# Kernel optimization log

Hardware: AMD Instinct MI355X
Metric: run time of the kernel (lower is better)

The kernel has to match this reference:

```python
import jax, jax.numpy as jnp
import numpy as np

EPS_BN = 1e-5
EPS_LN = 1e-5
OUT_H, OUT_W = 256, 256


def conv2d(x, w, b, pad):
    y = jax.lax.conv_general_dilated(x, w, (1, 1), [(pad, pad), (pad, pad)],
                                     dimension_numbers=('NCHW', 'OIHW', 'NCHW'))
    return y + b[None, :, None, None]


def leaky(x):
    return jnp.where(x >= 0, x, 0.2 * x)


def bn_eval(x, g, b):
    # fresh BatchNorm2d in eval mode: running_mean=0, running_var=1
    scale = g / jnp.sqrt(1.0 + EPS_BN)
    return x * scale[None, :, None, None] + b[None, :, None, None]


def resize_bilinear(x, oh, ow):
    # align_corners=True bilinear, separable gathers
    n, c, h, w = x.shape
    sy = jnp.arange(oh, dtype=x.dtype) * ((h - 1) / (oh - 1))
    sx = jnp.arange(ow, dtype=x.dtype) * ((w - 1) / (ow - 1))
    y0 = jnp.clip(jnp.floor(sy).astype(jnp.int32), 0, h - 2)
    x0 = jnp.clip(jnp.floor(sx).astype(jnp.int32), 0, w - 2)
    fy = (sy - y0.astype(x.dtype))[None, None, :, None]
    fx = (sx - x0.astype(x.dtype))[None, None, None, :]
    top = x[:, :, y0, :] * (1 - fy) + x[:, :, y0 + 1, :] * fy        # (n,c,oh,w)
    out = top[:, :, :, x0] * (1 - fx) + top[:, :, :, x0 + 1] * fx    # (n,c,oh,ow)
    return out


def layernorm(x, g, b):
    mu = jnp.mean(x, axis=-1, keepdims=True)
    var = jnp.mean((x - mu) ** 2, axis=-1, keepdims=True)
    return (x - mu) * jax.lax.rsqrt(var + EPS_LN) * g + b


def setup_inputs() -> dict:
    key = jax.random.key(0)
    ks = iter(jax.random.split(key, 64))

    def rn(shape, scale=0.05):
        return (jax.random.normal(next(ks), shape, dtype=jnp.float32) * scale)

    inp = {'x': jax.random.normal(next(ks), (8, 64, 128, 128), dtype=jnp.float32)}
    inp.update(
        r_c7a_w=rn((16, 64, 7, 7)), r_c7a_b=jnp.zeros((16,), jnp.float32),
        r_c1_w=rn((16, 16, 1, 1)), r_c1_b=jnp.zeros((16,), jnp.float32),
        r_bn1_g=1.0 + rn((16,), 0.1), r_bn1_b=jnp.zeros((16,), jnp.float32),
        rb_c1_w=rn((16, 16, 3, 3)), rb_c1_b=jnp.zeros((16,), jnp.float32),
        rb_bn1_g=1.0 + rn((16,), 0.1), rb_bn1_b=jnp.zeros((16,), jnp.float32),
        rb_c2_w=rn((16, 16, 3, 3)), rb_c2_b=jnp.zeros((16,), jnp.float32),
        rb_bn2_g=1.0 + rn((16,), 0.1), rb_bn2_b=jnp.zeros((16,), jnp.float32),
        r_c3_w=rn((16, 16, 3, 3)), r_c3_b=jnp.zeros((16,), jnp.float32),
        r_bn2_g=1.0 + rn((16,), 0.1), r_bn2_b=jnp.zeros((16,), jnp.float32),
        r_c7b_w=rn((64, 16, 7, 7)), r_c7b_b=jnp.zeros((64,), jnp.float32),
        a_k_w=rn((1, 64, 1, 1)), a_k_b=jnp.zeros((1,), jnp.float32),
        a_q_w=rn((1, 64, 1, 1)), a_q_b=jnp.zeros((1,), jnp.float32),
        a_v_w=rn((8, 64, 1, 1)), a_v_b=jnp.zeros((8,), jnp.float32),
        a_r_w=rn((64, 8, 1, 1)), a_r_b=jnp.zeros((64,), jnp.float32),
        t_ln_g=jnp.ones((64,), jnp.float32), t_ln_b=jnp.zeros((64,), jnp.float32),
        t_fc1_w=rn((64, 64)), t_fc1_b=jnp.zeros((64,), jnp.float32),
        t_fc2_w=rn((64, 64)), t_fc2_b=jnp.zeros((64,), jnp.float32),
    )
    return inp


def reference(x, r_c7a_w, r_c7a_b, r_c1_w, r_c1_b, r_bn1_g, r_bn1_b,
              rb_c1_w, rb_c1_b, rb_bn1_g, rb_bn1_b, rb_c2_w, rb_c2_b,
              rb_bn2_g, rb_bn2_b, r_c3_w, r_c3_b, r_bn2_g, r_bn2_b,
              r_c7b_w, r_c7b_b, a_k_w, a_k_b, a_q_w, a_q_b, a_v_w, a_v_b,
              a_r_w, a_r_b, t_ln_g, t_ln_b, t_fc1_w, t_fc1_b, t_fc2_w, t_fc2_b):
    # ---- Resizer ----
    identity = resize_bilinear(x, OUT_H, OUT_W)
    y = leaky(conv2d(x, r_c7a_w, r_c7a_b, 3))
    y = bn_eval(leaky(conv2d(y, r_c1_w, r_c1_b, 0)), r_bn1_g, r_bn1_b)
    y = resize_bilinear(y, OUT_H, OUT_W)
    conv_identity = y
    z = leaky(bn_eval(conv2d(y, rb_c1_w, rb_c1_b, 1), rb_bn1_g, rb_bn1_b))
    z = bn_eval(conv2d(z, rb_c2_w, rb_c2_b, 1), rb_bn2_g, rb_bn2_b) + y
    z = bn_eval(conv2d(z, r_c3_w, r_c3_b, 1), r_bn2_g, r_bn2_b) + conv_identity
    out = conv2d(z, r_c7b_w, r_c7b_b, 3) + identity

    # ---- EfficientAttention (key_channels=1, head_count=1, value_channels=8) ----
    n, c, h, w = out.shape
    hw = h * w
    k = conv2d(out, a_k_w, a_k_b, 0).reshape(n, 1, hw)
    q = conv2d(out, a_q_w, a_q_b, 0).reshape(n, 1, hw)
    v = conv2d(out, a_v_w, a_v_b, 0).reshape(n, 8, hw)
    key = jax.nn.softmax(k, axis=2)            # softmax over spatial positions
    query = jax.nn.softmax(q, axis=1)          # size-1 channel axis -> ones (faithful)
    context = jnp.einsum('nkp,nvp->nkv', key, v)          # (n,1,8)
    att = jnp.einsum('nkv,nkp->nvp', context, query)      # (n,8,hw)
    out = conv2d(att.reshape(n, 8, h, w), a_r_w, a_r_b, 0) + out

    # ---- TransformerBlock (identity conv, 1 encoder: x + MLP(LN(x))) ----
    t = out.reshape(n, c, hw).transpose(2, 0, 1)          # (hw, n, c)
    tn = layernorm(t, t_ln_g, t_ln_b)
    m = jax.nn.gelu(tn @ t_fc1_w.T + t_fc1_b, approximate=False) @ t_fc2_w.T + t_fc2_b
    t = t + m
    return t.transpose(1, 2, 0).reshape(n, c, h, w)
```

## Files before the change

### kernel.cpp

```cpp
#include <hip/hip_runtime.h>
#include <math.h>

#define DI __device__ __forceinline__
#define HW128 (128*128)
#define HW256 (256*256)

__device__ const float BN_RS = 0.9999950000374997f;

DI float leakyf(float x){ return x >= 0.f ? x : 0.2f*x; }

DI unsigned short f2bf(float f){
    unsigned u = __float_as_uint(f);
    return (unsigned short)((u + 0x7fffu + ((u >> 16) & 1u)) >> 16);
}
DI void unpack2(unsigned u, float& lo, float& hi){
    lo = __uint_as_float(u << 16);
    hi = __uint_as_float(u & 0xffff0000u);
}
DI void load8(const uint4* s, size_t idx, unsigned* d){
    uint4 t0 = s[idx], t1 = s[idx + 1];
    d[0]=t0.x; d[1]=t0.y; d[2]=t0.z; d[3]=t0.w;
    d[4]=t1.x; d[5]=t1.y; d[6]=t1.z; d[7]=t1.w;
}

typedef __attribute__((ext_vector_type(8))) short short8v;
typedef __attribute__((ext_vector_type(4))) float float4v;

__global__ __launch_bounds__(256) void prepack(
    const float* __restrict__ w7a, const float* __restrict__ w1,
    const float* __restrict__ w3a, const float* __restrict__ b3a, const float* __restrict__ g3a, const float* __restrict__ be3a,
    const float* __restrict__ w3b, const float* __restrict__ b3b, const float* __restrict__ g3b, const float* __restrict__ be3b,
    const float* __restrict__ w3c, const float* __restrict__ b3c, const float* __restrict__ g3c, const float* __restrict__ be3c,
    const float* __restrict__ w7b, const float* __restrict__ fc1w, const float* __restrict__ fc2w,
    unsigned short* __restrict__ p7aB, float* __restrict__ p1,
    float* __restrict__ q3a, float* __restrict__ q3b, float* __restrict__ q3c,
    unsigned short* __restrict__ w3aB, unsigned short* __restrict__ w3bB, unsigned short* __restrict__ w3cB,
    unsigned short* __restrict__ pwB,
    unsigned short* __restrict__ pwT1, unsigned short* __restrict__ pwT2)
{
    int i = blockIdx.x * 256 + threadIdx.x;
    if (i < 57344) {
        int g = i / 14336, rem = i - g*14336;
        int ks = rem >> 9, oc = (rem >> 5) & 15, k = rem & 31;
        int ky = ks >> 2, kx = ((ks & 3) << 1) + (k >> 4), ic = g*16 + (k & 15);
        p7aB[i] = (kx < 7) ? f2bf(w7a[(oc*64 + ic)*49 + ky*7 + kx]) : (unsigned short)0;
    }
    if (i < 57344) {
        int ks = i >> 11, oc = (i >> 5) & 63, k = i & 31;
        int ky = ks >> 2, kx = ((ks & 3) << 1) + (k >> 4), ic = k & 15;
        pwB[i] = (kx < 7) ? f2bf(w7b[((oc*16 + ic)*7 + ky)*7 + kx]) : (unsigned short)0;
    }
    if (i < 3072) {
        int ks = i >> 9, oc = (i >> 5) & 15, k = i & 31;
        int ky = ks >> 1, kx = ((ks & 1) << 1) + (k >> 4), ic = k & 15;
        if (kx < 3) {
            int src = (oc*16 + ic)*9 + ky*3 + kx;
            w3aB[i] = f2bf(w3a[src] * (g3a[oc]*BN_RS));
            w3bB[i] = f2bf(w3b[src] * (g3b[oc]*BN_RS));
            w3cB[i] = f2bf(w3c[src] * (g3c[oc]*BN_RS));
        } else {
            w3aB[i] = 0; w3bB[i] = 0; w3cB[i] = 0;
        }
    }
    if (i < 256) { int oc = i & 15, ic = i >> 4; p1[i] = w1[oc*16 + ic]; }
    if (i < 16) {
        q3a[i] = b3a[i]*(g3a[i]*BN_RS) + be3a[i];
        q3b[i] = b3b[i]*(g3b[i]*BN_RS) + be3b[i];
        q3c[i] = b3c[i]*(g3c[i]*BN_RS) + be3c[i];
    }
    if (i < 4096) { pwT1[i] = f2bf(fc1w[i]); pwT2[i] = f2bf(fc2w[i]); }
}

__global__ __launch_bounds__(256) void x_to_ci(
    const float* __restrict__ x, unsigned short* __restrict__ xci)
{
    int idx = blockIdx.x*256 + threadIdx.x;
    int p = idx & 16383, gn = idx >> 14;
    int g = gn & 3, n = gn >> 2;
    const float* xb = x + (size_t)(n*64 + g*16)*HW128 + p;
    unsigned q[8];
#pragma unroll
    for (int h = 0; h < 8; ++h) {
        float a0 = xb[(size_t)(2*h)*HW128];
        float a1 = xb[(size_t)(2*h + 1)*HW128];
        q[h] = (unsigned)f2bf(a0) | ((unsigned)f2bf(a1) << 16);
    }
    uint4* dst = (uint4*)xci + (size_t)idx*2;
    dst[0] = make_uint4(q[0], q[1], q[2], q[3]);
    dst[1] = make_uint4(q[4], q[5], q[6], q[7]);
}

__global__ __launch_bounds__(256) void conv7a_mfma(
    const unsigned short* __restrict__ xci,
    const unsigned short* __restrict__ pw,
    const float* __restrict__ b7a, const float* __restrict__ p1,
    const float* __restrict__ b1, const float* __restrict__ bng,
    const float* __restrict__ bnb, unsigned short* __restrict__ y2ci)
{
    __shared__ __align__(16) unsigned char lds[17408];
    unsigned short* tile = (unsigned short*)lds;
    float* P16 = (float*)lds;

    const int tid = threadIdx.x;
    const int n = blockIdx.z, ox = blockIdx.x*16, oy = blockIdx.y*16;
    const int w = tid >> 6, l = tid & 63, lg = l >> 4, ln = l & 15;

    float4v acc[4];
#pragma unroll
    for (int mi = 0; mi < 4; ++mi) acc[mi] = (float4v){0.f,0.f,0.f,0.f};

    const uint4* xc4 = (const uint4*)xci;
    uint4* tl4 = (uint4*)tile;
    const short8v* Bb = (const short8v*)pw;

    for (int g = 0; g < 4; ++g) {
        __syncthreads();
        for (int u = tid; u < 1056; u += 256) {
            int r = u / 48, s = u - r*48;
            int y = oy + r - 3, xcol = ox + (s >> 1) - 3;
            uint4 v = make_uint4(0u,0u,0u,0u);
            if (y >= 0 && y < 128 && xcol >= 0 && xcol < 128)
                v = xc4[((size_t)(n*4 + g)*16384 + y*128 + xcol)*2 + (s & 1)];
            tl4[u] = v;
        }
        __syncthreads();
        for (int ks = 0; ks < 28; ++ks) {
            const int ky = ks >> 2, kxp = (ks & 3) << 1;
            short8v b = Bb[(g*28 + ks)*64 + ln*4 + lg];
            short8v a[4];
#pragma unroll
            for (int mi = 0; mi < 4; ++mi) {
                int row = (4*w + mi) + ky;
                a[mi] = *(const short8v*)(tile + (row*24 + ln + kxp)*16 + lg*8);
            }
#pragma unroll
            for (int mi = 0; mi < 4; ++mi)
                acc[mi] = __builtin_amdgcn_mfma_f32_16x16x32_bf16(a[mi], b, acc[mi], 0, 0, 0);
        }
    }
    __syncthreads();
    const float bo = b7a[ln];
#pragma unroll
    for (int mi = 0; mi < 4; ++mi)
#pragma unroll
        for (int r = 0; r < 4; ++r)
            P16[((4*w + mi)*16 + lg*4 + r)*17 + ln] = leakyf(acc[mi][r] + bo);
    __syncthreads();
    const int py = tid >> 4, pxx = tid & 15;
    float lv[16];
#pragma unroll
    for (int ic = 0; ic < 16; ++ic) lv[ic] = P16[tid*17 + ic];
    float u16[16];
#pragma unroll
    for (int o = 0; o < 16; ++o) {
        float u = b1[o];
#pragma unroll
        for (int ic = 0; ic < 16; ++ic) u += lv[ic] * p1[ic*16 + o];
        u = leakyf(u);
        u16[o] = u * (bng[o]*BN_RS) + bnb[o];
    }
    const int p = (oy + py)*128 + ox + pxx;
    unsigned q[8];
#pragma unroll
    for (int h = 0; h < 8; ++h)
        q[h] = (unsigned)f2bf(u16[2*h]) | ((unsigned)f2bf(u16[2*h+1]) << 16);
    uint4* dst = (uint4*)y2ci + (size_t)(n*16384 + p)*2;
    dst[0] = make_uint4(q[0], q[1], q[2], q[3]);
    dst[1] = make_uint4(q[4], q[5], q[6], q[7]);
}

__global__ __launch_bounds__(256) void resize_ci(
    const unsigned short* __restrict__ y2ci, unsigned short* __restrict__ yci)
{
    const int n = blockIdx.z;
    const int ox = blockIdx.x*16 + threadIdx.x;
    const int oy = blockIdx.y*16 + threadIdx.y;
    float sy = oy * (127.f/255.f), sx = ox * (127.f/255.f);
    int y0 = min((int)sy, 126), x0 = min((int)sx, 126);
    float fy = sy - y0, fx = sx - x0;
    const uint4* src = (const uint4*)y2ci;
    size_t i00 = ((size_t)n*16384 + y0*128 + x0)*2;
    unsigned A00[8], A01[8], A10[8], A11[8];
    load8(src, i00,       A00);
    load8(src, i00 + 2,   A01);
    load8(src, i00 + 256, A10);
    load8(src, i00 + 258, A11);
    unsigned q[8];
#pragma unroll
    for (int h = 0; h < 8; ++h) {
        float l00, h00, l01, h01, l10, h10, l11, h11;
        unpack2(A00[h], l00, h00); unpack2(A01[h], l01, h01);
        unpack2(A10[h], l10, h10); unpack2(A11[h], l11, h11);
        float lo = (l00*(1.f-fx) + l01*fx)*(1.f-fy) + (l10*(1.f-fx) + l11*fx)*fy;
        float hi = (h00*(1.f-fx) + h01*fx)*(1.f-fy) + (h10*(1.f-fx) + h11*fx)*fy;
        q[h] = (unsigned)f2bf(lo) | ((unsigned)f2bf(hi) << 16);
    }
    uint4* dst = (uint4*)yci + ((size_t)n*65536 + oy*256 + ox)*2;
    dst[0] = make_uint4(q[0], q[1], q[2], q[3]);
    dst[1] = make_uint4(q[4], q[5], q[6], q[7]);
}

template<int MODE>
__global__ __launch_bounds__(256) void conv3_mfma(
    const unsigned short* __restrict__ in_ci,
    const unsigned short* __restrict__ wB, const float* __restrict__ q3,
    const unsigned short* __restrict__ res_ci,
    unsigned short* __restrict__ out_ci)
{
    __shared__ __align__(16) unsigned char lds[17408];
    unsigned short* tile = (unsigned short*)lds;
    float* P16 = (float*)lds;

    const int tid = threadIdx.x;
    const int n = blockIdx.z, ox = blockIdx.x*16, oy = blockIdx.y*16;
    const int w = tid >> 6, l = tid & 63, lg = l >> 4, ln = l & 15;

    const uint4* zc = (const uint4*)in_ci;
    uint4* tl4 = (uint4*)tile;
    for (int u = tid; u < 720; u += 256) {
        int r = u / 40, s = u - r*40;
        int y = oy + r - 1, xcol = ox + (s >> 1) - 1;
        uint4 v = make_uint4(0u,0u,0u,0u);
        if (y >= 0 && y < 256 && xcol >= 0 && xcol < 256)
            v = zc[((size_t)n*65536 + y*256 + xcol)*2 + (s & 1)];
        tl4[u] = v;
    }
    __syncthreads();

    float4v acc[4];
#pragma unroll
    for (int mi = 0; mi < 4; ++mi) acc[mi] = (float4v){0.f,0.f,0.f,0.f};
    const short8v* Bb = (const short8v*)wB;
#pragma unroll
    for (int ks = 0; ks < 6; ++ks) {
        const int ky = ks >> 1, kxp = (ks & 1) << 1;
        short8v b = Bb[(ks*16 + ln)*4 + lg];
        short8v a[4];
#pragma unroll
        for (int mi = 0; mi < 4; ++mi) {
            int row = (4*w + mi) + ky;
            a[mi] = *(const short8v*)(tile + (row*20 + ln + kxp)*16 + lg*8);
        }
#pragma unroll
        for (int mi = 0; mi < 4; ++mi)
            acc[mi] = __builtin_amdgcn_mfma_f32_16x16x32_bf16(a[mi], b, acc[mi], 0, 0, 0);
    }
    __syncthreads();
#pragma unroll
    for (int mi = 0; mi < 4; ++mi)
#pragma unroll
        for (int r = 0; r < 4; ++r)
            P16[((4*w + mi)*16 + lg*4 + r)*17 + ln] = acc[mi][r];
    __syncthreads();

    const int py = tid >> 4, pxx = tid & 15;
    const int p = (oy + py)*256 + ox + pxx;
    float u16[16];
#pragma unroll
    for (int o = 0; o < 16; ++o) u16[o] = P16[tid*17 + o] + q3[o];
    if (MODE == 0) {
#pragma unroll
        for (int o = 0; o < 16; ++o) u16[o] = leakyf(u16[o]);
    } else {
        unsigned R[8];
        load8((const uint4*)res_ci, ((size_t)n*65536 + p)*2, R);
#pragma unroll
        for (int h = 0; h < 8; ++h) {
            float lo, hi; unpack2(R[h], lo, hi);
            u16[2*h] += lo; u16[2*h+1] += hi;
        }
    }
    unsigned q[8];
#pragma unroll
    for (int h = 0; h < 8; ++h)
        q[h] = (unsigned)f2bf(u16[2*h]) | ((unsigned)f2bf(u16[2*h+1]) << 16);
    uint4* dst = (uint4*)out_ci + ((size_t)n*65536 + p)*2;
    dst[0] = make_uint4(q[0], q[1], q[2], q[3]);
    dst[1] = make_uint4(q[4], q[5], q[6], q[7]);
}

__global__ __launch_bounds__(256) void conv7b_mfma(
    const unsigned short* __restrict__ z_ci,
    const unsigned short* __restrict__ pwB,
    const unsigned short* __restrict__ xci,
    const float* __restrict__ bias,
    const float* __restrict__ akw, const float* __restrict__ akb,
    float* __restrict__ out0, float* __restrict__ kbuf)
{
    __shared__ __align__(16) unsigned char lds[17408 + 14400];
    unsigned short* tile = (unsigned short*)lds;
    float* P16 = (float*)lds;
    unsigned short* xt16 = (unsigned short*)(lds + 17408);

    const int tid = threadIdx.x;
    const int n = blockIdx.z, ox = blockIdx.x*16, oy = blockIdx.y*16;
    const float SC = 127.f/255.f;
    const int ybase = (int)(oy*SC), xbase = (int)(ox*SC);

    const uint4* zc = (const uint4*)z_ci;
    uint4* tl4 = (uint4*)tile;
    for (int u = tid; u < 1056; u += 256) {
        int r = u / 48, s = u - r*48;
        int y = oy + r - 3, xcol = ox + (s >> 1) - 3;
        uint4 v = make_uint4(0u, 0u, 0u, 0u);
        if (y >= 0 && y < 256 && xcol >= 0 && xcol < 256)
            v = zc[(size_t)((n*256 + y)*256 + xcol)*2 + (s & 1)];
        tl4[u] = v;
    }
    const uint4* xc4 = (const uint4*)xci;
    uint4* xt4 = (uint4*)xt16;
    for (int u = tid; u < 900; u += 256) {
        int p = u / 9, s = u - p*9;
        uint4 v = make_uint4(0u, 0u, 0u, 0u);
        if (s < 8) {
            int g = s >> 1, half = s & 1;
            int r = p / 10, c = p - r*10;
            int y = ybase + r, xcc = xbase + c;
            if (y < 128 && xcc < 128)
                v = xc4[((size_t)(n*4 + g)*16384 + y*128 + xcc)*2 + half];
        }
        xt4[u] = v;
    }
    __syncthreads();

    const int w = tid >> 6, l = tid & 63;
    const int lg = l >> 4, ln = l & 15;
    float4v acc[4][4];
#pragma unroll
    for (int mi = 0; mi < 4; ++mi)
#pragma unroll
        for (int nt = 0; nt < 4; ++nt)
            acc[mi][nt] = (float4v){0.f, 0.f, 0.f, 0.f};

    const short8v* Bb = (const short8v*)pwB;
    for (int ks = 0; ks < 28; ++ks) {
        const int ky = ks >> 2, kxp = (ks & 3) << 1;
        short8v a[4], b[4];
#pragma unroll
        for (int mi = 0; mi < 4; ++mi) {
            int row = (4*w + mi) + ky;
            a[mi] = *(const short8v*)(tile + (row*24 + ln + kxp)*16 + lg*8);
        }
#pragma unroll
        for (int nt = 0; nt < 4; ++nt)
            b[nt] = Bb[ks*256 + nt*64 + ln*4 + lg];
#pragma unroll
        for (int mi = 0; mi < 4; ++mi)
#pragma unroll
            for (int nt = 0; nt < 4; ++nt)
                acc[mi][nt] = __builtin_amdgcn_mfma_f32_16x16x32_bf16(
                    a[mi], b[nt], acc[mi][nt], 0, 0, 0);
    }

    const int py = tid >> 4, pxx = tid & 15;
    const int ohy = oy + py, ohx = ox + pxx;
    float sy = ohy*SC, sx = ohx*SC;
    int y0 = min((int)sy, 126), x0 = min((int)sx, 126);
    float fy = sy - y0, fx = sx - x0;
    const int ly = y0 - ybase, lx = x0 - xbase;
    const int p = ohy*256 + ohx;
    const uint4* xt4c = (const uint4*)xt16;
    const size_t q00 = (size_t)(ly*10 + lx)*9;
    float kacc = akb[0];

    for (int nt = 0; nt < 4; ++nt) {
        __syncthreads();
#pragma unroll
        for (int mi = 0; mi < 4; ++mi)
#pragma unroll
            for (int r = 0; r < 4; ++r)
                P16[((4*w + mi)*16 + lg*4 + r)*17 + ln] = acc[mi][nt][r];
        __syncthreads();
        unsigned A00[8], A01[8], A10[8], A11[8];
        size_t qb = q00 + nt*2;
        load8(xt4c, qb,      A00);
        load8(xt4c, qb + 9,  A01);
        load8(xt4c, qb + 90, A10);
        load8(xt4c, qb + 99, A11);
        float u16[16];
#pragma unroll
        for (int h = 0; h < 8; ++h) {
            float l00, h00, l01, h01, l10, h10, l11, h11;
            unpack2(A00[h], l00, h00); unpack2(A01[h], l01, h01);
            unpack2(A10[h], l10, h10); unpack2(A11[h], l11, h11);
            u16[2*h]   = (l00*(1.f-fx) + l01*fx)*(1.f-fy) + (l10*(1.f-fx) + l11*fx)*fy;
            u16[2*h+1] = (h00*(1.f-fx) + h01*fx)*(1.f-fy) + (h10*(1.f-fx) + h11*fx)*fy;
        }
#pragma unroll
        for (int o = 0; o < 16; ++o) {
            int oc = nt*16 + o;
            float u = P16[tid*17 + o] + bias[oc] + u16[o];
            out0[(size_t)(n*64 + oc)*HW256 + p] = u;
            kacc += akw[oc] * u;
        }
    }
    kbuf[n*65536 + p] = kacc;
}

__global__ __launch_bounds__(256) void softmax_part(
    const float* __restrict__ kb, float* __restrict__ pst)
{
    __shared__ float red[4];
    __shared__ float bcast;
    const int pc = blockIdx.x, n = blockIdx.y, tid = threadIdx.x;
    const float* kp = kb + n*65536 + pc*8192;
    float mx = -3.0e38f;
    for (int i = tid; i < 8192; i += 256) mx = fmaxf(mx, kp[i]);
#pragma unroll
    for (int off = 1; off < 64; off <<= 1) mx = fmaxf(mx, __shfl_xor(mx, off));
    int w = tid >> 6, l = tid & 63;
    if (l == 0) red[w] = mx;
    __syncthreads();
    if (tid == 0) bcast = fmaxf(fmaxf(red[0], red[1]), fmaxf(red[2], red[3]));
    __syncthreads();
    float BM = bcast;
    float s = 0.f;
    for (int i = tid; i < 8192; i += 256) s += __expf(kp[i] - BM);
#pragma unroll
    for (int off = 1; off < 64; off <<= 1) s += __shfl_xor(s, off);
    __syncthreads();
    if (l == 0) red[w] = s;
    __syncthreads();
    if (tid == 0) {
        pst[(n*8 + pc)*2]     = BM;
        pst[(n*8 + pc)*2 + 1] = red[0] + red[1] + red[2] + red[3];
    }
}

__global__ __launch_bounds__(64) void softmax_comb(
    const float* __restrict__ pst, float* __restrict__ st)
{
    int tid = threadIdx.x;
    if (tid < 8) {
        int n = tid;
        float MX = -3.0e38f;
        for (int c = 0; c < 8; ++c) MX = fmaxf(MX, pst[(n*8 + c)*2]);
        float S = 0.f;
        for (int c = 0; c < 8; ++c)
            S += pst[(n*8 + c)*2 + 1] * __expf(pst[(n*8 + c)*2] - MX);
        st[n] = MX; st[8 + n] = 1.f / S;
    }
}

__global__ __launch_bounds__(256) void att_wsum(
    const float* __restrict__ out0, const float* __restrict__ kb,
    const float* __restrict__ st, float* __restrict__ Sp)
{
    const int cg = blockIdx.x, pc = blockIdx.y, n = blockIdx.z, c0 = cg*8;
    const float mx = st[n];
    const float* kp = kb + n*65536 + pc*16384;
    const float* base = out0 + (size_t)(n*64 + c0)*HW256 + pc*16384;
    float acc[8];
#pragma unroll
    for (int c = 0; c < 8; ++c) acc[c] = 0.f;
    for (int p = threadIdx.x; p < 16384; p += 256) {
        float e = __expf(kp[p] - mx);
#pragma unroll
        for (int c = 0; c < 8; ++c) acc[c] += e * base[c*HW256 + p];
    }
#pragma unroll
    for (int c = 0; c < 8; ++c)
#pragma unroll
        for (int off = 1; off < 64; off <<= 1) acc[c] += __shfl_xor(acc[c], off);
    __shared__ float red[4][8];
    int w = threadIdx.x >> 6, l = threadIdx.x & 63;
    if (l == 0) {
#pragma unroll
        for (int c = 0; c < 8; ++c) red[w][c] = acc[c];
    }
    __syncthreads();
    if (threadIdx.x < 8)
        Sp[n*256 + pc*64 + c0 + threadIdx.x] =
            red[0][threadIdx.x] + red[1][threadIdx.x] + red[2][threadIdx.x] + red[3][threadIdx.x];
}

__global__ __launch_bounds__(512) void ctx_addc(
    const float* __restrict__ Sp, const float* __restrict__ st,
    const float* __restrict__ avw, const float* __restrict__ avb,
    const float* __restrict__ arw, const float* __restrict__ arb,
    float* __restrict__ addc)
{
    __shared__ float ctx[8][8];
    const int tid = threadIdx.x;
    if (tid < 64) {
        int n = tid >> 3, vc = tid & 7;
        float s = 0.f;
        for (int c = 0; c < 64; ++c) {
            float Sv = Sp[n*256 + c] + Sp[n*256 + 64 + c]
                     + Sp[n*256 + 128 + c] + Sp[n*256 + 192 + c];
            s += avw[vc*64 + c] * Sv;
        }
        ctx[n][vc] = s * st[8 + n] + avb[vc];
    }
    __syncthreads();
    int n = tid >> 6, c = tid & 63;
    float a = arb[c];
#pragma unroll
    for (int vc = 0; vc < 8; ++vc) a += arw[c*8 + vc] * ctx[n][vc];
    addc[n*64 + c] = a;
}

__global__ __launch_bounds__(256) void transformer_mfma(
    float* __restrict__ out0, const float* __restrict__ addc,
    const float* __restrict__ lng, const float* __restrict__ lnb,
    const unsigned short* __restrict__ W1b, const float* __restrict__ fc1b,
    const unsigned short* __restrict__ W2b, const float* __restrict__ fc2b)
{
    __shared__ __align__(16) unsigned char lds[17408 + 9216];
    float*          Xt = (float*)lds;
    unsigned short* Xb = (unsigned short*)(lds + 17408);
    unsigned short* Hb = Xb;

    const int tid = threadIdx.x;
    const int n = blockIdx.x >> 10;
    const int p0 = (blockIdx.x & 1023) << 6;
    const float* ac = addc + n*64;

#pragma unroll
    for (int k = 0; k < 4; ++k) {
        int v = k*256 + tid;
        int c = v >> 4, i4 = (v & 15) << 2;
        float4v q = *(const float4v*)(out0 + (size_t)(n*64 + c)*HW256 + p0 + i4);
        float a = ac[c];
#pragma unroll
        for (int r = 0; r < 4; ++r) q[r] += a;
        *(float4v*)&Xt[c*68 + i4] = q;
    }
    __syncthreads();

    if (tid < 64) {
        float t[64];
#pragma unroll
        for (int c = 0; c < 64; ++c) t[c] = Xt[c*68 + tid];
        float mu = 0.f;
#pragma unroll
        for (int c = 0; c < 64; ++c) mu += t[c];
        mu *= (1.f/64.f);
        float var = 0.f;
#pragma unroll
        for (int c = 0; c < 64; ++c) { float d = t[c] - mu; var += d*d; }
        var *= (1.f/64.f);
        float rs = rsqrtf(var + 1e-5f);
#pragma unroll
        for (int c8 = 0; c8 < 8; ++c8) {
            short8v pk;
#pragma unroll
            for (int e = 0; e < 8; ++e) {
                int c = c8*8 + e;
                pk[e] = (short)f2bf((t[c] - mu)*rs*lng[c] + lnb[c]);
            }
            *(short8v*)&Xb[tid*72 + c8*8] = pk;
        }
    }
    __syncthreads();

    const int w = tid >> 6, l = tid & 63, lg = l >> 4, ln = l & 15;

    float4v acc1[4];
#pragma unroll
    for (int nt = 0; nt < 4; ++nt) acc1[nt] = (float4v){0.f,0.f,0.f,0.f};
#pragma unroll
    for (int kk = 0; kk < 2; ++kk) {
        short8v a = *(const short8v*)&Xb[(w*16 + ln)*72 + kk*32 + lg*8];
        short8v b[4];
#pragma unroll
        for (int nt = 0; nt < 4; ++nt)
            b[nt] = *(const short8v*)&W1b[(nt*16 + ln)*64 + kk*32 + lg*8];
#pragma unroll
        for (int nt = 0; nt < 4; ++nt)
            acc1[nt] = __builtin_amdgcn_mfma_f32_16x16x32_bf16(a, b[nt], acc1[nt], 0, 0, 0);
    }
    __syncthreads();
#pragma unroll
    for (int nt = 0; nt < 4; ++nt) {
        int j = nt*16 + ln;
        float bj = fc1b[j];
#pragma unroll
        for (int r = 0; r < 4; ++r) {
            int token = w*16 + lg*4 + r;
            float m = acc1[nt][r] + bj;
            float g = 0.5f*m*(1.f + erff(m*0.70710678118654752f));
            Hb[token*72 + j] = f2bf(g);
        }
    }
    __syncthreads();

    float4v acc2[4];
#pragma unroll
    for (int nt = 0; nt < 4; ++nt) acc2[nt] = (float4v){0.f,0.f,0.f,0.f};
#pragma unroll
    for (int kk = 0; kk < 2; ++kk) {
        short8v a = *(const short8v*)&Hb[(w*16 + ln)*72 + kk*32 + lg*8];
        short8v b[4];
#pragma unroll
        for (int nt = 0; nt < 4; ++nt)
            b[nt] = *(const short8v*)&W2b[(nt*16 + ln)*64 + kk*32 + lg*8];
#pragma unroll
        for (int nt = 0; nt < 4; ++nt)
            acc2[nt] = __builtin_amdgcn_mfma_f32_16x16x32_bf16(a, b[nt], acc2[nt], 0, 0, 0);
    }
#pragma unroll
    for (int nt = 0; nt < 4; ++nt) {
        int c = nt*16 + ln;
        int tb = w*16 + lg*4;
        float add = fc2b[c];
        float4v t4 = *(const float4v*)&Xt[c*68 + tb];
        float* dst = out0 + (size_t)(n*64 + c)*HW256 + p0 + tb;
        float4v o;
#pragma unroll
        for (int r = 0; r < 4; ++r) o[r] = t4[r] + acc2[nt][r] + add;
        *(float4v*)dst = o;
    }
}

extern "C" void kernel_launch(void* const* d_in, const int* in_sizes, int n_in,
                              void* d_out, int out_size, void* d_ws, size_t ws_size,
                              hipStream_t stream)
{
    (void)in_sizes; (void)n_in; (void)out_size; (void)ws_size;
    const float* x    = (const float*)d_in[0];
    const float* w7a  = (const float*)d_in[1];
    const float* b7a  = (const float*)d_in[2];
    const float* w1   = (const float*)d_in[3];
    const float* b1   = (const float*)d_in[4];
    const float* g1   = (const float*)d_in[5];
    const float* be1  = (const float*)d_in[6];
    const float* w3a  = (const float*)d_in[7];
    const float* b3a  = (const float*)d_in[8];
    const float* g3a  = (const float*)d_in[9];
    const float* be3a = (const float*)d_in[10];
    const float* w3b  = (const float*)d_in[11];
    const float* b3b  = (const float*)d_in[12];
    const float* g3b  = (const float*)d_in[13];
    const float* be3b = (const float*)d_in[14];
    const float* w3c  = (const float*)d_in[15];
    const float* b3c  = (const float*)d_in[16];
    const float* g3c  = (const float*)d_in[17];
    const float* be3c = (const float*)d_in[18];
    const float* w7b  = (const float*)d_in[19];
    const float* b7b  = (const float*)d_in[20];
    const float* akw  = (const float*)d_in[21];
    const float* akb  = (const float*)d_in[22];
    const float* avw  = (const float*)d_in[25];
    const float* avb  = (const float*)d_in[26];
    const float* arw  = (const float*)d_in[27];
    const float* arb  = (const float*)d_in[28];
    const float* lng  = (const float*)d_in[29];
    const float* lnb  = (const float*)d_in[30];
    const float* fc1w = (const float*)d_in[31];
    const float* fc1b = (const float*)d_in[32];
    const float* fc2w = (const float*)d_in[33];
    const float* fc2b = (const float*)d_in[34];

    float* ws = (float*)d_ws;
    unsigned short* y2ci = (unsigned short*)ws;
    unsigned short* yci  = (unsigned short*)(ws + 1048576);
    unsigned short* z1ci = (unsigned short*)(ws + 1048576 + 4194304);
    unsigned short* z2ci = (unsigned short*)(ws + 1048576 + 2*4194304);
    unsigned short* xci  = (unsigned short*)(ws + 1048576 + 3*4194304);
    float* o_k   = ws + 1048576 + 4*4194304;
    float* o_st  = o_k + 524288;
    float* o_pst = o_st + 64;
    float* o_Sp  = o_pst + 128;
    float* o_ad  = o_Sp + 2048;
    unsigned short* p7aB = (unsigned short*)(o_ad + 512);
    float* p1   = o_ad + 512 + 28672;
    float* q3a  = p1 + 256;
    float* q3b  = q3a + 16;
    float* q3c  = q3b + 16;
    unsigned short* w3aB = (unsigned short*)(q3c + 16);
    unsigned short* w3bB = w3aB + 3072;
    unsigned short* w3cB = w3bB + 3072;
    unsigned short* pwB  = w3cB + 3072;
    unsigned short* pwT1 = pwB + 57344;
    unsigned short* pwT2 = pwT1 + 4096;

    unsigned short* z3ci = z1ci;
    float* out0 = (float*)d_out;

    prepack<<<224, 256, 0, stream>>>(w7a, w1, w3a,b3a,g3a,be3a, w3b,b3b,g3b,be3b,
                                     w3c,b3c,g3c,be3c, w7b, fc1w, fc2w,
                                     p7aB, p1, q3a, q3b, q3c, w3aB, w3bB, w3cB,
                                     pwB, pwT1, pwT2);
    x_to_ci<<<2048, 256, 0, stream>>>(x, xci);
    conv7a_mfma<<<dim3(8,8,8), 256, 0, stream>>>(xci, p7aB, b7a, p1, b1, g1, be1, y2ci);
    resize_ci<<<dim3(16,16,8), dim3(16,16), 0, stream>>>(y2ci, yci);
    conv3_mfma<0><<<dim3(16,16,8), 256, 0, stream>>>(yci,  w3aB, q3a, nullptr, z1ci);
    conv3_mfma<1><<<dim3(16,16,8), 256, 0, stream>>>(z1ci, w3bB, q3b, yci,     z2ci);
    conv3_mfma<1><<<dim3(16,16,8), 256, 0, stream>>>(z2ci, w3cB, q3c, yci,     z3ci);
    conv7b_mfma<<<dim3(16,16,8), 256, 0, stream>>>(z3ci, pwB, xci, b7b, akw, akb, out0, o_k);
    softmax_part<<<dim3(8,8), 256, 0, stream>>>(o_k, o_pst);
    softmax_comb<<<1, 64, 0, stream>>>(o_pst, o_st);
    att_wsum<<<dim3(8,4,8), 256, 0, stream>>>(out0, o_k, o_st, o_Sp);
    ctx_addc<<<1, 512, 0, stream>>>(o_Sp, o_st, avw, avb, arw, arb, o_ad);
    transformer_mfma<<<8192, 256, 0, stream>>>(out0, o_ad, lng, lnb, pwT1, fc1b, pwT2, fc2b);
}
```

Measured before the change: 322.7 us.

## Write conv7b epilogue directly from MFMA accumulators and cut transformer register use

The conv7b epilogue no longer stages accumulators through LDS with per-tile barriers. Each lane now computes the bilinear identity for its own accumulator elements, writes float4 rows straight to global memory, and reduces the attention-key dot product with wave shuffles. The transformer kernel gets a launch-bounds occupancy hint, and LayerNorm switches to single-pass sum/sum-of-squares statistics that re-read LDS instead of holding 64 floats in registers. This trades barriers and LDS round trips for scalar bf16 LDS gathers, plus a small loss of numerical robustness in the variance.

```diff
diff --git a/kernel.cpp b/kernel.cpp
--- a/kernel.cpp
+++ b/kernel.cpp
@@ -13,6 +13,7 @@
     unsigned u = __float_as_uint(f);
     return (unsigned short)((u + 0x7fffu + ((u >> 16) & 1u)) >> 16);
 }
+DI float bf2f(unsigned short us){ return __uint_as_float((unsigned)us << 16); }
 DI void unpack2(unsigned u, float& lo, float& hi){
     lo = __uint_as_float(u << 16);
     hi = __uint_as_float(u & 0xffff0000u);
@@ -289,7 +290,6 @@
 {
     __shared__ __align__(16) unsigned char lds[17408 + 14400];
     unsigned short* tile = (unsigned short*)lds;
-    float* P16 = (float*)lds;
     unsigned short* xt16 = (unsigned short*)(lds + 17408);
 
     const int tid = threadIdx.x;
@@ -352,49 +352,66 @@
                     a[mi], b[nt], acc[mi][nt], 0, 0, 0);
     }
 
-    const int py = tid >> 4, pxx = tid & 15;
-    const int ohy = oy + py, ohx = ox + pxx;
-    float sy = ohy*SC, sx = ohx*SC;
-    int y0 = min((int)sy, 126), x0 = min((int)sx, 126);
-    float fy = sy - y0, fx = sx - x0;
-    const int ly = y0 - ybase, lx = x0 - xbase;
-    const int p = ohy*256 + ohx;
-    const uint4* xt4c = (const uint4*)xt16;
-    const size_t q00 = (size_t)(ly*10 + lx)*9;
-    float kacc = akb[0];
-
+    float akwv[4], bv[4];
+#pragma unroll
     for (int nt = 0; nt < 4; ++nt) {
-        __syncthreads();
-#pragma unroll
-        for (int mi = 0; mi < 4; ++mi)
-#pragma unroll
-            for (int r = 0; r < 4; ++r)
-                P16[((4*w + mi)*16 + lg*4 + r)*17 + ln] = acc[mi][nt][r];
-        __syncthreads();
-        unsigned A00[8], A01[8], A10[8], A11[8];
-        size_t qb = q00 + nt*2;
-        load8(xt4c, qb,      A00);
-        load8(xt4c, qb + 9,  A01);
-        load8(xt4c, qb + 90, A10);
-        load8(xt4c, qb + 99, A11);
-        float u16[16];
-#pragma unroll
-        for (int h = 0; h < 8; ++h) {
-            float l00, h00, l01, h01, l10, h10, l11, h11;
-            unpack2(A00[h], l00, h00); unpack2(A01[h], l01, h01);
-            unpack2(A10[h], l10, h10); unpack2(A11[h], l11, h11);
-            u16[2*h]   = (l00*(1.f-fx) + l01*fx)*(1.f-fy) + (l10*(1.f-fx) + l11*fx)*fy;
-            u16[2*h+1] = (h00*(1.f-fx) + h01*fx)*(1.f-fy) + (h10*(1.f-fx) + h11*fx)*fy;
-        }
-#pragma unroll
-        for (int o = 0; o < 16; ++o) {
-            int oc = nt*16 + o;
-            float u = P16[tid*17 + o] + bias[oc] + u16[o];
-            out0[(size_t)(n*64 + oc)*HW256 + p] = u;
-            kacc += akw[oc] * u;
-        }
-    }
-    kbuf[n*65536 + p] = kacc;
+        akwv[nt] = akw[nt*16 + ln];
+        bv[nt]   = bias[nt*16 + ln];
+    }
+    float kp[4][4];
+#pragma unroll
+    for (int mi = 0; mi < 4; ++mi)
+#pragma unroll
+        for (int r = 0; r < 4; ++r) kp[mi][r] = 0.f;
+
+#pragma unroll
+    for (int mi = 0; mi < 4; ++mi) {
+        const int yy = oy + 4*w + mi;
+        float syy = yy*SC; int y0 = min((int)syy, 126); float fy = syy - y0;
+        const int ly = y0 - ybase;
+        float fxr[4]; int lxr[4];
+#pragma unroll
+        for (int r = 0; r < 4; ++r) {
+            int px = ox + lg*4 + r;
+            float sxx = px*SC; int x0 = min((int)sxx, 126);
+            fxr[r] = sxx - x0; lxr[r] = x0 - xbase;
+        }
+#pragma unroll
+        for (int nt = 0; nt < 4; ++nt) {
+            const int oc = nt*16 + ln;
+            float4v o;
+#pragma unroll
+            for (int r = 0; r < 4; ++r) {
+                int b00 = (ly*10 + lxr[r])*72 + oc;
+                float v00 = bf2f(xt16[b00]);
+                float v01 = bf2f(xt16[b00 + 72]);
+                float v10 = bf2f(xt16[b00 + 720]);
+                float v11 = bf2f(xt16[b00 + 792]);
+                float idv = (v00*(1.f-fxr[r]) + v01*fxr[r])*(1.f-fy)
+                          + (v10*(1.f-fxr[r]) + v11*fxr[r])*fy;
+                float u = acc[mi][nt][r] + bv[nt] + idv;
+                o[r] = u;
+                kp[mi][r] += akwv[nt]*u;
+            }
+            float* dst = out0 + (size_t)(n*64 + oc)*HW256 + yy*256 + ox + lg*4;
+            *(float4v*)dst = o;
+        }
+    }
+    float kw = 0.f;
+#pragma unroll
+    for (int mi = 0; mi < 4; ++mi)
+#pragma unroll
+        for (int r = 0; r < 4; ++r) {
+            float v = kp[mi][r];
+            v += __shfl_xor(v, 1); v += __shfl_xor(v, 2);
+            v += __shfl_xor(v, 4); v += __shfl_xor(v, 8);
+            if (ln == mi*4 + r) kw = v;
+        }
+    {
+        const int yy = oy + 4*w + (ln >> 2);
+        const int px = ox + lg*4 + (ln & 3);
+        kbuf[n*65536 + yy*256 + px] = kw + akb[0];
+    }
 }
 
 __global__ __launch_bounds__(256) void softmax_part(
@@ -500,7 +517,7 @@
     addc[n*64 + c] = a;
 }
 
-__global__ __launch_bounds__(256) void transformer_mfma(
+__global__ __launch_bounds__(256, 6) void transformer_mfma(
     float* __restrict__ out0, const float* __restrict__ addc,
     const float* __restrict__ lng, const float* __restrict__ lnb,
     const unsigned short* __restrict__ W1b, const float* __restrict__ fc1b,
@@ -529,17 +546,14 @@
     __syncthreads();
 
     if (tid < 64) {
-        float t[64];
-#pragma unroll
-        for (int c = 0; c < 64; ++c) t[c] = Xt[c*68 + tid];
-        float mu = 0.f;
-#pragma unroll
-        for (int c = 0; c < 64; ++c) mu += t[c];
-        mu *= (1.f/64.f);
-        float var = 0.f;
-#pragma unroll
-        for (int c = 0; c < 64; ++c) { float d = t[c] - mu; var += d*d; }
-        var *= (1.f/64.f);
+        float sum = 0.f, sq = 0.f;
+#pragma unroll
+        for (int c = 0; c < 64; ++c) {
+            float v = Xt[c*68 + tid];
+            sum += v; sq += v*v;
+        }
+        float mu = sum * (1.f/64.f);
+        float var = fmaxf(sq * (1.f/64.f) - mu*mu, 0.f);
         float rs = rsqrtf(var + 1e-5f);
 #pragma unroll
         for (int c8 = 0; c8 < 8; ++c8) {
@@ -547,7 +561,8 @@
 #pragma unroll
             for (int e = 0; e < 8; ++e) {
                 int c = c8*8 + e;
-                pk[e] = (short)f2bf((t[c] - mu)*rs*lng[c] + lnb[c]);
+                float v = Xt[c*68 + tid];
+                pk[e] = (short)f2bf((v - mu)*rs*lng[c] + lnb[c]);
             }
             *(short8v*)&Xb[tid*72 + c8*8] = pk;
         }
```

Result: slower. 424.6 us (+31.6%).
